# Optimization experiments

Hardware: AMD Instinct MI355X
Metric: run time of the kernel (lower is better)

## Reference

```python
import jax, jax.numpy as jnp
import numpy as np

B, D, H = 32768, 1024, 8
LN_EPS = 1e-5


def setup_inputs() -> dict:
    key = jax.random.key(0)
    ks = jax.random.split(key, 12)
    w = lambda k, shape: (jax.random.normal(k, shape, dtype=jnp.float32) * 0.02)
    inp = {
        "graph_embedding": jax.random.normal(ks[0], (B, D), dtype=jnp.float32),
        "smiles_embedding": jax.random.normal(ks[1], (B, D), dtype=jnp.float32),
        "num_heads": H,
        # cross_attn_graph_to_smiles params (torch MHA: in_proj [3D,D] split q/k/v, out_proj [D,D])
        "Wq_gs": w(ks[2], (D, D)), "Wk_gs": w(ks[3], (D, D)), "Wv_gs": w(ks[4], (D, D)),
        "bq_gs": jnp.zeros((D,), jnp.float32), "bk_gs": jnp.zeros((D,), jnp.float32), "bv_gs": jnp.zeros((D,), jnp.float32),
        "Wo_gs": w(ks[5], (D, D)), "bo_gs": jnp.zeros((D,), jnp.float32),
        # cross_attn_smiles_to_graph params
        "Wq_sg": w(ks[6], (D, D)), "Wk_sg": w(ks[7], (D, D)), "Wv_sg": w(ks[8], (D, D)),
        "bq_sg": jnp.zeros((D,), jnp.float32), "bk_sg": jnp.zeros((D,), jnp.float32), "bv_sg": jnp.zeros((D,), jnp.float32),
        "Wo_sg": w(ks[9], (D, D)), "bo_sg": jnp.zeros((D,), jnp.float32),
        # LayerNorms
        "ln_g_gamma": jnp.ones((D,), jnp.float32), "ln_g_beta": jnp.zeros((D,), jnp.float32),
        "ln_s_gamma": jnp.ones((D,), jnp.float32), "ln_s_beta": jnp.zeros((D,), jnp.float32),
        # Gate: Linear(2D -> D) then sigmoid
        "Wg": w(ks[10], (D, 2 * D)), "bg": jnp.zeros((D,), jnp.float32),
    }
    return inp


def _layernorm(x, gamma, beta):
    mu = jnp.mean(x, axis=-1, keepdims=True)
    var = jnp.mean(jnp.square(x - mu), axis=-1, keepdims=True)
    return (x - mu) * jax.lax.rsqrt(var + LN_EPS) * gamma + beta


def _mha_len1(kv, Wv, bv, Wo, bo):
    # seq_len=1 cross-attention: softmax over a single key is identically 1,
    # so output == out_proj(v_proj(kv)). q/k projections contribute nothing
    # (and have exactly zero gradient), matching torch's math.
    v = kv @ Wv.T + bv
    return v @ Wo.T + bo


def reference(graph_embedding, smiles_embedding, num_heads,
              Wq_gs, Wk_gs, Wv_gs, bq_gs, bk_gs, bv_gs, Wo_gs, bo_gs,
              Wq_sg, Wk_sg, Wv_sg, bq_sg, bk_sg, bv_sg, Wo_sg, bo_sg,
              ln_g_gamma, ln_g_beta, ln_s_gamma, ln_s_beta, Wg, bg):
    # dropout p=0 / eval mode -> identity
    attn_g2s = _mha_len1(smiles_embedding, Wv_gs, bv_gs, Wo_gs, bo_gs)  # graph queries smiles
    attn_s2g = _mha_len1(graph_embedding, Wv_sg, bv_sg, Wo_sg, bo_sg)   # smiles queries graph
    fused_graph = _layernorm(graph_embedding + attn_g2s, ln_g_gamma, ln_g_beta)
    fused_smiles = _layernorm(smiles_embedding + attn_s2g, ln_s_gamma, ln_s_beta)
    gate_in = jnp.concatenate([fused_graph, fused_smiles], axis=1)  # [B, 2D]
    gate_weight = jax.nn.sigmoid(gate_in @ Wg.T + bg)               # [B, D]
    fused_feature = gate_weight * fused_graph + (1.0 - gate_weight) * fused_smiles
    return fused_feature, gate_weight
```

## Files before the change

kernel.cpp:

```cpp
#include <hip/hip_runtime.h>

#define BROWS 32768
#define DDIM 1024

typedef __bf16 bf16x8v __attribute__((ext_vector_type(8)));
typedef float f32x4v __attribute__((ext_vector_type(4)));

__device__ __forceinline__ float bf2f(unsigned short u) {
  union { unsigned int i; float f; } w; w.i = ((unsigned int)u) << 16; return w.f;
}
__device__ __forceinline__ unsigned short f2bf(float f) {
  union { float f; unsigned int i; } w; w.f = f;
  w.i += 0x7fffu + ((w.i >> 16) & 1u);
  return (unsigned short)(w.i >> 16);
}

__device__ __forceinline__ void gl_lds16(const void* g, void* l) {
  __builtin_amdgcn_global_load_lds((const __attribute__((address_space(1))) void*)g,
                                   (__attribute__((address_space(3))) void*)l, 16, 0, 0);
}

__device__ __forceinline__ int xcd_swz(int bid, int nwg) {
  return (bid & 7) * (nwg >> 3) + (bid >> 3);
}

__device__ __forceinline__ int swzc(int row, int col) {
  return (col & ~63) | ((col & 63) ^ ((row & 7) << 3));
}

__global__ __launch_bounds__(256) void cvt_x(const float* __restrict__ g,
                                             const float* __restrict__ s,
                                             unsigned short* __restrict__ xg,
                                             unsigned short* __restrict__ xs) {
  const size_t N = (size_t)BROWS * DDIM;
  size_t i = ((size_t)blockIdx.x * 256 + threadIdx.x) * 4;
  const float* src = (i < N) ? g : s;
  unsigned short* dst = (i < N) ? xg : xs;
  size_t off = (i < N) ? i : i - N;
  int row = (int)(off >> 10), col = (int)(off & 1023);
  float4 v = *(const float4*)&src[off];
  union { uint2 q; unsigned short h[4]; } u;
  u.h[0] = f2bf(v.x); u.h[1] = f2bf(v.y); u.h[2] = f2bf(v.z); u.h[3] = f2bf(v.w);
  *(uint2*)&dst[(size_t)row * DDIM + swzc(row, col)] = u.q;
}

__global__ __launch_bounds__(256) void cvt_wg(const float* __restrict__ s,
                                              unsigned short* __restrict__ d) {
  int i = (blockIdx.x * 256 + threadIdx.x) * 4;
  int row = i >> 11, col = i & 2047;
  float4 v = *(const float4*)&s[i];
  union { uint2 q; unsigned short h[4]; } u;
  u.h[0] = f2bf(v.x); u.h[1] = f2bf(v.y); u.h[2] = f2bf(v.z); u.h[3] = f2bf(v.w);
  *(uint2*)&d[(size_t)row * 2048 + swzc(row, col)] = u.q;
}

__global__ __launch_bounds__(256) void bias_combine(
    const float* __restrict__ Wo_gs, const float* __restrict__ bv_gs,
    const float* __restrict__ bo_gs,
    const float* __restrict__ Wo_sg, const float* __restrict__ bv_sg,
    const float* __restrict__ bo_sg,
    float* __restrict__ bc_gs, float* __restrict__ bc_sg) {
  int gid = blockIdx.x * 256 + threadIdx.x;
  int pair = gid >> 10, j = gid & 1023;
  const float* Wo = pair ? Wo_sg : Wo_gs;
  const float* bv = pair ? bv_sg : bv_gs;
  const float* bo = pair ? bo_sg : bo_gs;
  float s = 0.f;
  for (int k = 0; k < DDIM; k += 4) {
    float4 w = *(const float4*)&Wo[(size_t)j * DDIM + k];
    float4 b = *(const float4*)&bv[k];
    s += w.x * b.x + w.y * b.y + w.z * b.z + w.w * b.w;
  }
  float* bc = pair ? bc_sg : bc_gs;
  bc[j] = s + bo[j];
}

__device__ __forceinline__ void stage_f32_32(const float* __restrict__ src, int ldk,
                                             int row0, int k0, unsigned short* lds, int tid) {
  const int sr = tid >> 2, sc = (tid & 3) * 8;
#pragma unroll
  for (int h = 0; h < 2; ++h) {
    const float* g = &src[(size_t)(row0 + h * 64 + sr) * ldk + k0 + sc];
    float4 va = ((const float4*)g)[0];
    float4 vb = ((const float4*)g)[1];
    union { uint4 q; unsigned short hh[8]; } u;
    u.hh[0] = f2bf(va.x); u.hh[1] = f2bf(va.y); u.hh[2] = f2bf(va.z); u.hh[3] = f2bf(va.w);
    u.hh[4] = f2bf(vb.x); u.hh[5] = f2bf(vb.y); u.hh[6] = f2bf(vb.z); u.hh[7] = f2bf(vb.w);
    *(uint4*)&lds[(h * 64 + sr) * 32 + sc] = u.q;
  }
}

__device__ __forceinline__ void mfma_tile32(const unsigned short* As, const unsigned short* Bs,
                                            int ab, int bb, f32x4v acc[4][4]) {
  const bf16x8v* Av = reinterpret_cast<const bf16x8v*>(As);
  const bf16x8v* Bv = reinterpret_cast<const bf16x8v*>(Bs);
  bf16x8v af[4], bfr[4];
#pragma unroll
  for (int m = 0; m < 4; ++m) af[m] = Av[ab + m * 64];
#pragma unroll
  for (int n = 0; n < 4; ++n) bfr[n] = Bv[bb + n * 64];
#pragma unroll
  for (int m = 0; m < 4; ++m)
#pragma unroll
    for (int n = 0; n < 4; ++n)
      acc[m][n] = __builtin_amdgcn_mfma_f32_16x16x32_bf16(af[m], bfr[n], acc[m][n], 0, 0, 0);
}

__global__ __launch_bounds__(256) void combine_kernel(
    const float* __restrict__ Wo_gs, const float* __restrict__ Wv_gs,
    const float* __restrict__ Wo_sg, const float* __restrict__ Wv_sg,
    unsigned short* __restrict__ Wc_gs, unsigned short* __restrict__ Wc_sg) {
  const int pair = blockIdx.y;
  const float* Wo = pair ? Wo_sg : Wo_gs;
  const float* Wv = pair ? Wv_sg : Wv_gs;
  unsigned short* Wc = pair ? Wc_sg : Wc_gs;
  const int mt = blockIdx.x >> 3, nt = blockIdx.x & 7;
  const int row0 = mt * 128, col0 = nt * 128;

  __shared__ __align__(16) unsigned short As[128 * 32];
  __shared__ __align__(16) unsigned short Bt[128 * 32];

  const int tid = threadIdx.x;
  const int lane = tid & 63, wave = tid >> 6;
  const int wr = wave >> 1, wc = wave & 1;
  const int lr = lane & 15, lk = lane >> 4;

  f32x4v acc[4][4] = {};
  const int ab = (wr * 64 + lr) * 4 + lk;
  const int bb = (wc * 64 + lr) * 4 + lk;

  for (int tt = 0; tt < 32; ++tt) {
    const int t0 = tt * 32;
    __syncthreads();
    stage_f32_32(Wo, DDIM, row0, t0, As, tid);
#pragma unroll
    for (int h = 0; h < 2; ++h) {
      int chunk = h * 256 + tid;
      int t = chunk >> 4;
      int c8 = (chunk & 15) * 8;
      const float* g = &Wv[(size_t)(t0 + t) * DDIM + col0 + c8];
      float4 va = ((const float4*)g)[0];
      float4 vb = ((const float4*)g)[1];
      float vv[8] = {va.x, va.y, va.z, va.w, vb.x, vb.y, vb.z, vb.w};
#pragma unroll
      for (int e = 0; e < 8; ++e) Bt[(c8 + e) * 32 + t] = f2bf(vv[e]);
    }
    __syncthreads();
    mfma_tile32(As, Bt, ab, bb, acc);
  }

#pragma unroll
  for (int n = 0; n < 4; ++n) {
    int col = col0 + wc * 64 + n * 16 + lr;
#pragma unroll
    for (int m = 0; m < 4; ++m) {
      int rbase = row0 + wr * 64 + m * 16 + lk * 4;
#pragma unroll
      for (int r = 0; r < 4; ++r)
        Wc[(size_t)(rbase + r) * DDIM + swzc(rbase + r, col)] = f2bf(acc[m][n][r]);
    }
  }
}


__global__ __launch_bounds__(256, 2) void gemm_branch8(
    const unsigned short* __restrict__ Xs_b, const unsigned short* __restrict__ Xg_b,
    const unsigned short* __restrict__ Wc_gs, const unsigned short* __restrict__ Wc_sg,
    const float* __restrict__ bc_gs, const float* __restrict__ bc_sg,
    unsigned short* __restrict__ Zg, unsigned short* __restrict__ Zs) {
  const int pair = blockIdx.y;
  const unsigned short* X = pair ? Xg_b : Xs_b;
  const unsigned short* residb = pair ? Xs_b : Xg_b;
  const unsigned short* Wc = pair ? Wc_sg : Wc_gs;
  const float* bc = pair ? bc_sg : bc_gs;
  unsigned short* Z = pair ? Zs : Zg;

  const int bid = xcd_swz(blockIdx.x, 2048);
  const int mt = bid >> 3, nt = bid & 7;
  const int row0 = mt * 128, col0 = nt * 128;
  const int NT = 16;

  __shared__ __align__(16) unsigned short As[3][128 * 64];
  __shared__ __align__(16) unsigned short Bs[2][128 * 64];

  const int tid = threadIdx.x;
  const int lane = tid & 63, wave = tid >> 6;
  const int wm = wave >> 1, wn = wave & 1;
  const int lr = lane & 15, lk = lane >> 4;

  f32x4v acc[4][4] = {};

  auto stageB = [&](int kt) {
#pragma unroll
    for (int r = 0; r < 4; ++r) {
      int idx = r * 2048 + tid * 8;
      int row = idx >> 6, ch = (tid & 7) * 8;
      gl_lds16(&Wc[(size_t)(col0 + row) * DDIM + kt * 64 + ch], &Bs[kt & 1][idx]);
    }
  };
  auto stageA = [&](int kt) {
    int slot = kt - (kt / 3) * 3;
#pragma unroll
    for (int r = 0; r < 4; ++r) {
      int idx = r * 2048 + tid * 8;
      int row = idx >> 6, ch = (tid & 7) * 8;
      gl_lds16(&X[(size_t)(row0 + row) * DDIM + kt * 64 + ch], &As[slot][idx]);
    }
  };

  stageB(0); stageA(0); stageA(1);

  for (int kt = 0; kt < NT; ++kt) {
    if (kt < NT - 1) asm volatile("s_waitcnt vmcnt(4)" ::: "memory");
    else             asm volatile("s_waitcnt vmcnt(0)" ::: "memory");
    asm volatile("s_barrier" ::: "memory");
    if (kt + 1 < NT) stageB(kt + 1);
    if (kt + 2 < NT) stageA(kt + 2);

    const unsigned short* Ak = As[kt - (kt / 3) * 3];
    const unsigned short* Bk = Bs[kt & 1];
    bf16x8v bv[4][2], av[4][2];
#pragma unroll
    for (int n = 0; n < 4; ++n)
#pragma unroll
      for (int s = 0; s < 2; ++s) {
        int row = wn * 64 + n * 16 + lr;
        bv[n][s] = *(const bf16x8v*)&Bk[row * 64 + (((s * 4 + lk) ^ (row & 7)) * 8)];
      }
#pragma unroll
    for (int m = 0; m < 4; ++m)
#pragma unroll
      for (int s = 0; s < 2; ++s) {
        int row = wm * 64 + m * 16 + lr;
        av[m][s] = *(const bf16x8v*)&Ak[row * 64 + (((s * 4 + lk) ^ (row & 7)) * 8)];
      }
    __builtin_amdgcn_s_setprio(1);
#pragma unroll
    for (int s = 0; s < 2; ++s)
#pragma unroll
      for (int m = 0; m < 4; ++m)
#pragma unroll
        for (int n = 0; n < 4; ++n)
          acc[m][n] = __builtin_amdgcn_mfma_f32_16x16x32_bf16(av[m][s], bv[n][s],
                                                              acc[m][n], 0, 0, 0);
    __builtin_amdgcn_s_setprio(0);
  }

#pragma unroll
  for (int n = 0; n < 4; ++n) {
    int col = col0 + wn * 64 + n * 16 + lr;
    float bcv = bc[col];
#pragma unroll
    for (int m = 0; m < 4; ++m) {
      int rb = row0 + wm * 64 + m * 16 + lk * 4;
#pragma unroll
      for (int r = 0; r < 4; ++r) {
        int row = rb + r;
        size_t idx = (size_t)row * DDIM + swzc(row, col);
        Z[idx] = f2bf(acc[m][n][r] + bcv + bf2f(residb[idx]));
      }
    }
  }
}

__global__ __launch_bounds__(256, 2) void gemm_gate8(
    const unsigned short* __restrict__ fg, const unsigned short* __restrict__ fs,
    const unsigned short* __restrict__ WgB, const float* __restrict__ bg,
    float* __restrict__ out0, float* __restrict__ out1) {
  const int bid = xcd_swz(blockIdx.x, 2048);
  const int mt = bid >> 3, nt = bid & 7;
  const int row0 = mt * 128, col0 = nt * 128;
  const int NT = 32;

  __shared__ __align__(16) unsigned short As[3][128 * 64];
  __shared__ __align__(16) unsigned short Bs[2][128 * 64];

  const int tid = threadIdx.x;
  const int lane = tid & 63, wave = tid >> 6;
  const int wm = wave >> 1, wn = wave & 1;
  const int lr = lane & 15, lk = lane >> 4;

  f32x4v acc[4][4] = {};

  auto stageB = [&](int kt) {
#pragma unroll
    for (int r = 0; r < 4; ++r) {
      int idx = r * 2048 + tid * 8;
      int row = idx >> 6, ch = (tid & 7) * 8;
      gl_lds16(&WgB[(size_t)(col0 + row) * 2048 + kt * 64 + ch], &Bs[kt & 1][idx]);
    }
  };
  auto stageA = [&](int kt) {
    const unsigned short* asrc = (kt < 16) ? fg : fs;
    int ak0 = (kt & 15) * 64;
    int slot = kt - (kt / 3) * 3;
#pragma unroll
    for (int r = 0; r < 4; ++r) {
      int idx = r * 2048 + tid * 8;
      int row = idx >> 6, ch = (tid & 7) * 8;
      gl_lds16(&asrc[(size_t)(row0 + row) * DDIM + ak0 + ch], &As[slot][idx]);
    }
  };

  stageB(0); stageA(0); stageA(1);

  for (int kt = 0; kt < NT; ++kt) {
    if (kt < NT - 1) asm volatile("s_waitcnt vmcnt(4)" ::: "memory");
    else             asm volatile("s_waitcnt vmcnt(0)" ::: "memory");
    asm volatile("s_barrier" ::: "memory");
    if (kt + 1 < NT) stageB(kt + 1);
    if (kt + 2 < NT) stageA(kt + 2);

    const unsigned short* Ak = As[kt - (kt / 3) * 3];
    const unsigned short* Bk = Bs[kt & 1];
    bf16x8v bv[4][2], av[4][2];
#pragma unroll
    for (int n = 0; n < 4; ++n)
#pragma unroll
      for (int s = 0; s < 2; ++s) {
        int row = wn * 64 + n * 16 + lr;
        bv[n][s] = *(const bf16x8v*)&Bk[row * 64 + (((s * 4 + lk) ^ (row & 7)) * 8)];
      }
#pragma unroll
    for (int m = 0; m < 4; ++m)
#pragma unroll
      for (int s = 0; s < 2; ++s) {
        int row = wm * 64 + m * 16 + lr;
        av[m][s] = *(const bf16x8v*)&Ak[row * 64 + (((s * 4 + lk) ^ (row & 7)) * 8)];
      }
    __builtin_amdgcn_s_setprio(1);
#pragma unroll
    for (int s = 0; s < 2; ++s)
#pragma unroll
      for (int m = 0; m < 4; ++m)
#pragma unroll
        for (int n = 0; n < 4; ++n)
          acc[m][n] = __builtin_amdgcn_mfma_f32_16x16x32_bf16(av[m][s], bv[n][s],
                                                              acc[m][n], 0, 0, 0);
    __builtin_amdgcn_s_setprio(0);
  }

#pragma unroll
  for (int n = 0; n < 4; ++n) {
    int col = col0 + wn * 64 + n * 16 + lr;
    float bgv = bg[col];
#pragma unroll
    for (int m = 0; m < 4; ++m) {
      int rb = row0 + wm * 64 + m * 16 + lk * 4;
#pragma unroll
      for (int r = 0; r < 4; ++r) {
        int row = rb + r;
        size_t sidx = (size_t)row * DDIM + swzc(row, col);
        size_t tidx = (size_t)row * DDIM + col;
        float g = 1.f / (1.f + __expf(-(acc[m][n][r] + bgv)));
        float a = bf2f(fg[sidx]), b = bf2f(fs[sidx]);
        out0[tidx] = g * a + (1.f - g) * b;
        out1[tidx] = g;
      }
    }
  }
}

__global__ __launch_bounds__(256) void ln_kernel(
    unsigned short* __restrict__ Z,
    const float* __restrict__ gam_g, const float* __restrict__ bet_g,
    const float* __restrict__ gam_s, const float* __restrict__ bet_s) {
  int row = blockIdx.x * 4 + (threadIdx.x >> 6);
  int lane = threadIdx.x & 63;
  const float* gam = (row < BROWS) ? gam_g : gam_s;
  const float* bet = (row < BROWS) ? bet_g : bet_s;
  unsigned short* zr = Z + (size_t)row * DDIM;

  uint4 v0 = *(const uint4*)(zr + lane * 8);
  uint4 v1 = *(const uint4*)(zr + 512 + lane * 8);
  const unsigned short* u0 = (const unsigned short*)&v0;
  const unsigned short* u1 = (const unsigned short*)&v1;
  float x[16];
  float s = 0.f, sq = 0.f;
#pragma unroll
  for (int e = 0; e < 8; ++e) { x[e] = bf2f(u0[e]); x[8 + e] = bf2f(u1[e]); }
#pragma unroll
  for (int i = 0; i < 16; ++i) { s += x[i]; sq += x[i] * x[i]; }
#pragma unroll
  for (int o = 32; o; o >>= 1) { s += __shfl_xor(s, o); sq += __shfl_xor(sq, o); }
  float mu = s * (1.f / 1024.f);
  float var = sq * (1.f / 1024.f) - mu * mu;
  float rstd = rsqrtf(var + 1e-5f);

  int lane2 = (lane & ~7) | ((lane & 7) ^ (row & 7));
  float4 g0 = *(const float4*)(gam + lane2 * 8);
  float4 g1 = *(const float4*)(gam + lane2 * 8 + 4);
  float4 g2 = *(const float4*)(gam + 512 + lane2 * 8);
  float4 g3 = *(const float4*)(gam + 512 + lane2 * 8 + 4);
  float4 b0 = *(const float4*)(bet + lane2 * 8);
  float4 b1 = *(const float4*)(bet + lane2 * 8 + 4);
  float4 b2 = *(const float4*)(bet + 512 + lane2 * 8);
  float4 b3 = *(const float4*)(bet + 512 + lane2 * 8 + 4);
  float gg[16] = {g0.x,g0.y,g0.z,g0.w,g1.x,g1.y,g1.z,g1.w,
                  g2.x,g2.y,g2.z,g2.w,g3.x,g3.y,g3.z,g3.w};
  float bb[16] = {b0.x,b0.y,b0.z,b0.w,b1.x,b1.y,b1.z,b1.w,
                  b2.x,b2.y,b2.z,b2.w,b3.x,b3.y,b3.z,b3.w};

  union { uint4 q; unsigned short h[8]; } o0, o1;
#pragma unroll
  for (int e = 0; e < 8; ++e) {
    o0.h[e] = f2bf((x[e] - mu) * rstd * gg[e] + bb[e]);
    o1.h[e] = f2bf((x[8 + e] - mu) * rstd * gg[8 + e] + bb[8 + e]);
  }
  *(uint4*)(zr + lane * 8) = o0.q;
  *(uint4*)(zr + 512 + lane * 8) = o1.q;
}

__global__ __launch_bounds__(256) void gemm_gate_f32(
    const unsigned short* __restrict__ fg, const unsigned short* __restrict__ fs,
    const float* __restrict__ Wg, const float* __restrict__ bg,
    float* __restrict__ out0, float* __restrict__ out1) {
  const int bid = xcd_swz(blockIdx.x, 2048);
  const int mt = bid >> 3, nt = bid & 7;
  const int row0 = mt * 128, col0 = nt * 128;

  __shared__ __align__(16) unsigned short As[128 * 64];
  __shared__ __align__(16) unsigned short Bsh[128 * 64];

  const int tid = threadIdx.x;
  const int lane = tid & 63, wave = tid >> 6;
  const int wr = wave >> 1, wc = wave & 1;
  const int lr = lane & 15, lk = lane >> 4;

  f32x4v acc[4][4] = {};

  for (int kt = 0; kt < 32; ++kt) {
    const unsigned short* Asrc = (kt < 16) ? fg : fs;
    const int k0 = (kt & 15) * 64;
    const int kw = kt * 64;
    __syncthreads();
#pragma unroll
    for (int h = 0; h < 4; ++h) {
      int row = h * 32 + (tid >> 3);
      gl_lds16(&Asrc[(size_t)(row0 + row) * DDIM + k0 + (tid & 7) * 8], &As[h * 2048 + tid * 8]);
    }
#pragma unroll
    for (int h = 0; h < 4; ++h) {
      int row = h * 32 + (tid >> 3), c16 = tid & 7;
      const float* gsrc = &Wg[(size_t)(col0 + row) * 2048 + kw + c16 * 8];
      float4 va = ((const float4*)gsrc)[0];
      float4 vb = ((const float4*)gsrc)[1];
      union { uint4 q; unsigned short hh[8]; } u;
      u.hh[0] = f2bf(va.x); u.hh[1] = f2bf(va.y); u.hh[2] = f2bf(va.z); u.hh[3] = f2bf(va.w);
      u.hh[4] = f2bf(vb.x); u.hh[5] = f2bf(vb.y); u.hh[6] = f2bf(vb.z); u.hh[7] = f2bf(vb.w);
      *(uint4*)&Bsh[(row * 8 + (c16 ^ (row & 7))) * 8] = u.q;
    }
    __syncthreads();
    const bf16x8v* Av = reinterpret_cast<const bf16x8v*>(As);
    const bf16x8v* Bv = reinterpret_cast<const bf16x8v*>(Bsh);
    const int xr = lr & 7;
#pragma unroll
    for (int s = 0; s < 2; ++s) {
      const int u = (s * 4 + lk) ^ xr;
      bf16x8v af[4], bfr[4];
#pragma unroll
      for (int m = 0; m < 4; ++m) af[m] = Av[(wr * 64 + m * 16 + lr) * 8 + u];
#pragma unroll
      for (int n = 0; n < 4; ++n) bfr[n] = Bv[(wc * 64 + n * 16 + lr) * 8 + u];
#pragma unroll
      for (int m = 0; m < 4; ++m)
#pragma unroll
        for (int n = 0; n < 4; ++n)
          acc[m][n] = __builtin_amdgcn_mfma_f32_16x16x32_bf16(af[m], bfr[n], acc[m][n], 0, 0, 0);
    }
  }

#pragma unroll
  for (int n = 0; n < 4; ++n) {
    int col = col0 + wc * 64 + n * 16 + lr;
    float bgv = bg[col];
#pragma unroll
    for (int m = 0; m < 4; ++m) {
      int rbase = row0 + wr * 64 + m * 16 + lk * 4;
#pragma unroll
      for (int r = 0; r < 4; ++r) {
        int row = rbase + r;
        size_t sidx = (size_t)row * DDIM + swzc(row, col);
        size_t tidx = (size_t)row * DDIM + col;
        float g = 1.f / (1.f + __expf(-(acc[m][n][r] + bgv)));
        float a = bf2f(fg[sidx]), b = bf2f(fs[sidx]);
        out0[tidx] = g * a + (1.f - g) * b;
        out1[tidx] = g;
      }
    }
  }
}

extern "C" void kernel_launch(void* const* d_in, const int* in_sizes, int n_in,
                              void* d_out, int out_size, void* d_ws, size_t ws_size,
                              hipStream_t stream) {
  const float* graph  = (const float*)d_in[0];
  const float* smiles = (const float*)d_in[1];
  const float* Wv_gs  = (const float*)d_in[5];
  const float* bv_gs  = (const float*)d_in[8];
  const float* Wo_gs  = (const float*)d_in[9];
  const float* bo_gs  = (const float*)d_in[10];
  const float* Wv_sg  = (const float*)d_in[13];
  const float* bv_sg  = (const float*)d_in[16];
  const float* Wo_sg  = (const float*)d_in[17];
  const float* bo_sg  = (const float*)d_in[18];
  const float* ln_gg  = (const float*)d_in[19];
  const float* ln_gb  = (const float*)d_in[20];
  const float* ln_sg  = (const float*)d_in[21];
  const float* ln_sb  = (const float*)d_in[22];
  const float* Wg     = (const float*)d_in[23];
  const float* bg     = (const float*)d_in[24];

  char* ob = (char*)d_out;
  unsigned short* Xg_b  = (unsigned short*)ob;
  unsigned short* Xs_b  = (unsigned short*)(ob + (64u << 20));
  unsigned short* Wc_gs = (unsigned short*)(ob + (128u << 20));
  unsigned short* Wc_sg = (unsigned short*)(ob + (130u << 20));
  float* bc_gs = (float*)(ob + (132u << 20));
  float* bc_sg = (float*)(ob + (132u << 20) + 4096);

  unsigned short* Zg = (unsigned short*)d_ws;
  unsigned short* Zs = Zg + (size_t)BROWS * DDIM;
  const bool fast = ws_size >= ((size_t)132 << 20);
  unsigned short* WgB = (unsigned short*)((char*)d_ws + ((size_t)128 << 20));

  float* out0 = (float*)d_out;
  float* out1 = out0 + (size_t)BROWS * DDIM;

  cvt_x<<<dim3(65536), dim3(256), 0, stream>>>(graph, smiles, Xg_b, Xs_b);
  bias_combine<<<dim3(8), dim3(256), 0, stream>>>(Wo_gs, bv_gs, bo_gs, Wo_sg, bv_sg, bo_sg,
                                                  bc_gs, bc_sg);
  combine_kernel<<<dim3(64, 2), dim3(256), 0, stream>>>(Wo_gs, Wv_gs, Wo_sg, Wv_sg,
                                                        Wc_gs, Wc_sg);
  if (fast) cvt_wg<<<dim3(2048), dim3(256), 0, stream>>>(Wg, WgB);
  gemm_branch8<<<dim3(2048, 2), dim3(256), 0, stream>>>(Xs_b, Xg_b, Wc_gs, Wc_sg,
                                                        bc_gs, bc_sg, Zg, Zs);
  ln_kernel<<<dim3(16384), dim3(256), 0, stream>>>(Zg, ln_gg, ln_gb, ln_sg, ln_sb);
  if (fast)
    gemm_gate8<<<dim3(2048), dim3(256), 0, stream>>>(Zg, Zs, WgB, bg, out0, out1);
  else
    gemm_gate_f32<<<dim3(2048), dim3(256), 0, stream>>>(Zg, Zs, Wg, bg, out0, out1);
}
```

Before: 706.3 us.

## Shrink GEMM K-tile to 32 with 4-deep A pipeline to raise occupancy

Both main GEMM kernels move from 64-wide K tiles to 32-wide K tiles. A now uses a 4-slot ring and B a 2-slot ring, which cuts LDS per block so three workgroups can fit per CU, and launch bounds change from 2 to 3. The global bf16 layout swizzle becomes a 32-column XOR over row&3 so global_load_lds can fill the smaller tiles directly, and every producer and consumer (convert kernels, LayerNorm, combine GEMM) is updated to match. The cost is twice as many barriers and waitcnt iterations, fewer MFMAs per barrier, and a weaker bank-conflict swizzle.

```diff
diff --git a/kernel.cpp b/kernel.cpp
--- a/kernel.cpp
+++ b/kernel.cpp
@@ -24,8 +24,8 @@
   return (bid & 7) * (nwg >> 3) + (bid >> 3);
 }
 
-__device__ __forceinline__ int swzc(int row, int col) {
-  return (col & ~63) | ((col & 63) ^ ((row & 7) << 3));
+__device__ __forceinline__ int swz32(int row, int col) {
+  return (col & ~31) | ((col & 31) ^ ((row & 3) << 3));
 }
 
 __global__ __launch_bounds__(256) void cvt_x(const float* __restrict__ g,
@@ -41,7 +41,7 @@
   float4 v = *(const float4*)&src[off];
   union { uint2 q; unsigned short h[4]; } u;
   u.h[0] = f2bf(v.x); u.h[1] = f2bf(v.y); u.h[2] = f2bf(v.z); u.h[3] = f2bf(v.w);
-  *(uint2*)&dst[(size_t)row * DDIM + swzc(row, col)] = u.q;
+  *(uint2*)&dst[(size_t)row * DDIM + swz32(row, col)] = u.q;
 }
 
 __global__ __launch_bounds__(256) void cvt_wg(const float* __restrict__ s,
@@ -51,7 +51,7 @@
   float4 v = *(const float4*)&s[i];
   union { uint2 q; unsigned short h[4]; } u;
   u.h[0] = f2bf(v.x); u.h[1] = f2bf(v.y); u.h[2] = f2bf(v.z); u.h[3] = f2bf(v.w);
-  *(uint2*)&d[(size_t)row * 2048 + swzc(row, col)] = u.q;
+  *(uint2*)&d[(size_t)row * 2048 + swz32(row, col)] = u.q;
 }
 
 __global__ __launch_bounds__(256) void bias_combine(
@@ -157,13 +157,13 @@
       int rbase = row0 + wr * 64 + m * 16 + lk * 4;
 #pragma unroll
       for (int r = 0; r < 4; ++r)
-        Wc[(size_t)(rbase + r) * DDIM + swzc(rbase + r, col)] = f2bf(acc[m][n][r]);
-    }
-  }
-}
-
-
-__global__ __launch_bounds__(256, 2) void gemm_branch8(
+        Wc[(size_t)(rbase + r) * DDIM + swz32(rbase + r, col)] = f2bf(acc[m][n][r]);
+    }
+  }
+}
+
+
+__global__ __launch_bounds__(256, 3) void gemm_branch8(
     const unsigned short* __restrict__ Xs_b, const unsigned short* __restrict__ Xg_b,
     const unsigned short* __restrict__ Wc_gs, const unsigned short* __restrict__ Wc_sg,
     const float* __restrict__ bc_gs, const float* __restrict__ bc_sg,
@@ -178,10 +178,10 @@
   const int bid = xcd_swz(blockIdx.x, 2048);
   const int mt = bid >> 3, nt = bid & 7;
   const int row0 = mt * 128, col0 = nt * 128;
-  const int NT = 16;
-
-  __shared__ __align__(16) unsigned short As[3][128 * 64];
-  __shared__ __align__(16) unsigned short Bs[2][128 * 64];
+  const int NT = 32;
+
+  __shared__ __align__(16) unsigned short As[4][128 * 32];
+  __shared__ __align__(16) unsigned short Bs[2][128 * 32];
 
   const int tid = threadIdx.x;
   const int lane = tid & 63, wave = tid >> 6;
@@ -192,57 +192,50 @@
 
   auto stageB = [&](int kt) {
 #pragma unroll
-    for (int r = 0; r < 4; ++r) {
-      int idx = r * 2048 + tid * 8;
-      int row = idx >> 6, ch = (tid & 7) * 8;
-      gl_lds16(&Wc[(size_t)(col0 + row) * DDIM + kt * 64 + ch], &Bs[kt & 1][idx]);
+    for (int j = 0; j < 2; ++j) {
+      int e = (j * 256 + tid) * 8;
+      int row = e >> 5, cp = e & 31;
+      gl_lds16(&Wc[(size_t)(col0 + row) * DDIM + kt * 32 + cp], &Bs[kt & 1][e]);
     }
   };
   auto stageA = [&](int kt) {
-    int slot = kt - (kt / 3) * 3;
-#pragma unroll
-    for (int r = 0; r < 4; ++r) {
-      int idx = r * 2048 + tid * 8;
-      int row = idx >> 6, ch = (tid & 7) * 8;
-      gl_lds16(&X[(size_t)(row0 + row) * DDIM + kt * 64 + ch], &As[slot][idx]);
+#pragma unroll
+    for (int j = 0; j < 2; ++j) {
+      int e = (j * 256 + tid) * 8;
+      int row = e >> 5, cp = e & 31;
+      gl_lds16(&X[(size_t)(row0 + row) * DDIM + kt * 32 + cp], &As[kt & 3][e]);
     }
   };
 
-  stageB(0); stageA(0); stageA(1);
+  stageB(0); stageA(0); stageA(1); stageA(2);
 
   for (int kt = 0; kt < NT; ++kt) {
-    if (kt < NT - 1) asm volatile("s_waitcnt vmcnt(4)" ::: "memory");
-    else             asm volatile("s_waitcnt vmcnt(0)" ::: "memory");
+    if (kt == 0)          asm volatile("s_waitcnt vmcnt(4)" ::: "memory");
+    else if (kt < NT - 2) asm volatile("s_waitcnt vmcnt(2)" ::: "memory");
+    else                  asm volatile("s_waitcnt vmcnt(0)" ::: "memory");
     asm volatile("s_barrier" ::: "memory");
     if (kt + 1 < NT) stageB(kt + 1);
-    if (kt + 2 < NT) stageA(kt + 2);
-
-    const unsigned short* Ak = As[kt - (kt / 3) * 3];
+    if (kt + 3 < NT) stageA(kt + 3);
+
+    const unsigned short* Ak = As[kt & 3];
     const unsigned short* Bk = Bs[kt & 1];
-    bf16x8v bv[4][2], av[4][2];
-#pragma unroll
-    for (int n = 0; n < 4; ++n)
-#pragma unroll
-      for (int s = 0; s < 2; ++s) {
-        int row = wn * 64 + n * 16 + lr;
-        bv[n][s] = *(const bf16x8v*)&Bk[row * 64 + (((s * 4 + lk) ^ (row & 7)) * 8)];
-      }
+    bf16x8v av[4], bv[4];
+#pragma unroll
+    for (int n = 0; n < 4; ++n) {
+      int row = wn * 64 + n * 16 + lr;
+      bv[n] = *(const bf16x8v*)&Bk[row * 32 + ((lk ^ (row & 3)) * 8)];
+    }
+#pragma unroll
+    for (int m = 0; m < 4; ++m) {
+      int row = wm * 64 + m * 16 + lr;
+      av[m] = *(const bf16x8v*)&Ak[row * 32 + ((lk ^ (row & 3)) * 8)];
+    }
+    __builtin_amdgcn_s_setprio(1);
 #pragma unroll
     for (int m = 0; m < 4; ++m)
 #pragma unroll
-      for (int s = 0; s < 2; ++s) {
-        int row = wm * 64 + m * 16 + lr;
-        av[m][s] = *(const bf16x8v*)&Ak[row * 64 + (((s * 4 + lk) ^ (row & 7)) * 8)];
-      }
-    __builtin_amdgcn_s_setprio(1);
-#pragma unroll
-    for (int s = 0; s < 2; ++s)
-#pragma unroll
-      for (int m = 0; m < 4; ++m)
-#pragma unroll
-        for (int n = 0; n < 4; ++n)
-          acc[m][n] = __builtin_amdgcn_mfma_f32_16x16x32_bf16(av[m][s], bv[n][s],
-                                                              acc[m][n], 0, 0, 0);
+      for (int n = 0; n < 4; ++n)
+        acc[m][n] = __builtin_amdgcn_mfma_f32_16x16x32_bf16(av[m], bv[n], acc[m][n], 0, 0, 0);
     __builtin_amdgcn_s_setprio(0);
   }
 
@@ -256,24 +249,24 @@
 #pragma unroll
       for (int r = 0; r < 4; ++r) {
         int row = rb + r;
-        size_t idx = (size_t)row * DDIM + swzc(row, col);
+        size_t idx = (size_t)row * DDIM + swz32(row, col);
         Z[idx] = f2bf(acc[m][n][r] + bcv + bf2f(residb[idx]));
       }
     }
   }
 }
 
-__global__ __launch_bounds__(256, 2) void gemm_gate8(
+__global__ __launch_bounds__(256, 3) void gemm_gate8(
     const unsigned short* __restrict__ fg, const unsigned short* __restrict__ fs,
     const unsigned short* __restrict__ WgB, const float* __restrict__ bg,
     float* __restrict__ out0, float* __restrict__ out1) {
   const int bid = xcd_swz(blockIdx.x, 2048);
   const int mt = bid >> 3, nt = bid & 7;
   const int row0 = mt * 128, col0 = nt * 128;
-  const int NT = 32;
-
-  __shared__ __align__(16) unsigned short As[3][128 * 64];
-  __shared__ __align__(16) unsigned short Bs[2][128 * 64];
+  const int NT = 64;
+
+  __shared__ __align__(16) unsigned short As[4][128 * 32];
+  __shared__ __align__(16) unsigned short Bs[2][128 * 32];
 
   const int tid = threadIdx.x;
   const int lane = tid & 63, wave = tid >> 6;
@@ -284,59 +277,52 @@
 
   auto stageB = [&](int kt) {
 #pragma unroll
-    for (int r = 0; r < 4; ++r) {
-      int idx = r * 2048 + tid * 8;
-      int row = idx >> 6, ch = (tid & 7) * 8;
-      gl_lds16(&WgB[(size_t)(col0 + row) * 2048 + kt * 64 + ch], &Bs[kt & 1][idx]);
+    for (int j = 0; j < 2; ++j) {
+      int e = (j * 256 + tid) * 8;
+      int row = e >> 5, cp = e & 31;
+      gl_lds16(&WgB[(size_t)(col0 + row) * 2048 + kt * 32 + cp], &Bs[kt & 1][e]);
     }
   };
   auto stageA = [&](int kt) {
-    const unsigned short* asrc = (kt < 16) ? fg : fs;
-    int ak0 = (kt & 15) * 64;
-    int slot = kt - (kt / 3) * 3;
-#pragma unroll
-    for (int r = 0; r < 4; ++r) {
-      int idx = r * 2048 + tid * 8;
-      int row = idx >> 6, ch = (tid & 7) * 8;
-      gl_lds16(&asrc[(size_t)(row0 + row) * DDIM + ak0 + ch], &As[slot][idx]);
+    const unsigned short* asrc = (kt < 32) ? fg : fs;
+    int ak0 = (kt & 31) * 32;
+#pragma unroll
+    for (int j = 0; j < 2; ++j) {
+      int e = (j * 256 + tid) * 8;
+      int row = e >> 5, cp = e & 31;
+      gl_lds16(&asrc[(size_t)(row0 + row) * DDIM + ak0 + cp], &As[kt & 3][e]);
     }
   };
 
-  stageB(0); stageA(0); stageA(1);
+  stageB(0); stageA(0); stageA(1); stageA(2);
 
   for (int kt = 0; kt < NT; ++kt) {
-    if (kt < NT - 1) asm volatile("s_waitcnt vmcnt(4)" ::: "memory");
-    else             asm volatile("s_waitcnt vmcnt(0)" ::: "memory");
+    if (kt == 0)          asm volatile("s_waitcnt vmcnt(4)" ::: "memory");
+    else if (kt < NT - 2) asm volatile("s_waitcnt vmcnt(2)" ::: "memory");
+    else                  asm volatile("s_waitcnt vmcnt(0)" ::: "memory");
     asm volatile("s_barrier" ::: "memory");
     if (kt + 1 < NT) stageB(kt + 1);
-    if (kt + 2 < NT) stageA(kt + 2);
-
-    const unsigned short* Ak = As[kt - (kt / 3) * 3];
+    if (kt + 3 < NT) stageA(kt + 3);
+
+    const unsigned short* Ak = As[kt & 3];
     const unsigned short* Bk = Bs[kt & 1];
-    bf16x8v bv[4][2], av[4][2];
-#pragma unroll
-    for (int n = 0; n < 4; ++n)
-#pragma unroll
-      for (int s = 0; s < 2; ++s) {
-        int row = wn * 64 + n * 16 + lr;
-        bv[n][s] = *(const bf16x8v*)&Bk[row * 64 + (((s * 4 + lk) ^ (row & 7)) * 8)];
-      }
+    bf16x8v av[4], bv[4];
+#pragma unroll
+    for (int n = 0; n < 4; ++n) {
+      int row = wn * 64 + n * 16 + lr;
+      bv[n] = *(const bf16x8v*)&Bk[row * 32 + ((lk ^ (row & 3)) * 8)];
+    }
+#pragma unroll
+    for (int m = 0; m < 4; ++m) {
+      int row = wm * 64 + m * 16 + lr;
+      av[m] = *(const bf16x8v*)&Ak[row * 32 + ((lk ^ (row & 3)) * 8)];
+    }
+    __builtin_amdgcn_s_setprio(1);
 #pragma unroll
     for (int m = 0; m < 4; ++m)
 #pragma unroll
-      for (int s = 0; s < 2; ++s) {
-        int row = wm * 64 + m * 16 + lr;
-        av[m][s] = *(const bf16x8v*)&Ak[row * 64 + (((s * 4 + lk) ^ (row & 7)) * 8)];
-      }
-    __builtin_amdgcn_s_setprio(1);
-#pragma unroll
-    for (int s = 0; s < 2; ++s)
-#pragma unroll
-      for (int m = 0; m < 4; ++m)
-#pragma unroll
-        for (int n = 0; n < 4; ++n)
-          acc[m][n] = __builtin_amdgcn_mfma_f32_16x16x32_bf16(av[m][s], bv[n][s],
-                                                              acc[m][n], 0, 0, 0);
+      for (int n = 0; n < 4; ++n)
+        acc[m][n] = __builtin_amdgcn_mfma_f32_16x16x32_bf16(av[m], bv[n], acc[m][n], 0, 0, 0);
     __builtin_amdgcn_s_setprio(0);
   }
 
@@ -350,7 +336,7 @@
 #pragma unroll
       for (int r = 0; r < 4; ++r) {
         int row = rb + r;
-        size_t sidx = (size_t)row * DDIM + swzc(row, col);
+        size_t sidx = (size_t)row * DDIM + swz32(row, col);
         size_t tidx = (size_t)row * DDIM + col;
         float g = 1.f / (1.f + __expf(-(acc[m][n][r] + bgv)));
         float a = bf2f(fg[sidx]), b = bf2f(fs[sidx]);
@@ -387,7 +373,7 @@
   float var = sq * (1.f / 1024.f) - mu * mu;
   float rstd = rsqrtf(var + 1e-5f);
 
-  int lane2 = (lane & ~7) | ((lane & 7) ^ (row & 7));
+  int lane2 = (lane & ~3) | ((lane & 3) ^ (row & 3));
   float4 g0 = *(const float4*)(gam + lane2 * 8);
   float4 g1 = *(const float4*)(gam + lane2 * 8 + 4);
   float4 g2 = *(const float4*)(gam + 512 + lane2 * 8);
@@ -448,20 +434,29 @@
       union { uint4 q; unsigned short hh[8]; } u;
       u.hh[0] = f2bf(va.x); u.hh[1] = f2bf(va.y); u.hh[2] = f2bf(va.z); u.hh[3] = f2bf(va.w);
       u.hh[4] = f2bf(vb.x); u.hh[5] = f2bf(vb.y); u.hh[6] = f2bf(vb.z); u.hh[7] = f2bf(vb.w);
-      *(uint4*)&Bsh[(row * 8 + (c16 ^ (row & 7))) * 8] = u.q;
+      int cst = (c16 & ~3) | ((c16 & 3) ^ (row & 3));
+      *(uint4*)&Bsh[(row * 8 + cst) * 8] = u.q;
     }
     __syncthreads();
     const bf16x8v* Av = reinterpret_cast<const bf16x8v*>(As);
     const bf16x8v* Bv = reinterpret_cast<const bf16x8v*>(Bsh);
-    const int xr = lr & 7;
 #pragma unroll
     for (int s = 0; s < 2; ++s) {
-      const int u = (s * 4 + lk) ^ xr;
       bf16x8v af[4], bfr[4];
 #pragma unroll
-      for (int m = 0; m < 4; ++m) af[m] = Av[(wr * 64 + m * 16 + lr) * 8 + u];
-#pragma unroll
-      for (int n = 0; n < 4; ++n) bfr[n] = Bv[(wc * 64 + n * 16 + lr) * 8 + u];
+      for (int m = 0; m < 4; ++m) {
+        int row = wr * 64 + m * 16 + lr;
+        int c = s * 4 + lk;
+        int u = (c & ~3) | ((c & 3) ^ (row & 3));
+        af[m] = Av[row * 8 + u];
+      }
+#pragma unroll
+      for (int n = 0; n < 4; ++n) {
+        int row = wc * 64 + n * 16 + lr;
+        int c = s * 4 + lk;
+        int u = (c & ~3) | ((c & 3) ^ (row & 3));
+        bfr[n] = Bv[row * 8 + u];
+      }
 #pragma unroll
       for (int m = 0; m < 4; ++m)
 #pragma unroll
@@ -480,7 +475,7 @@
 #pragma unroll
       for (int r = 0; r < 4; ++r) {
         int row = rbase + r;
-        size_t sidx = (size_t)row * DDIM + swzc(row, col);
+        size_t sidx = (size_t)row * DDIM + swz32(row, col);
         size_t tidx = (size_t)row * DDIM + col;
         float g = 1.f / (1.f + __expf(-(acc[m][n][r] + bgv)));
         float a = bf2f(fg[sidx]), b = bf2f(fs[sidx]);
```

Result: no change. 716.9 us (+1.5%).
